# Kernel tuning notes

Hardware: AMD Instinct MI355X
Metric: run time of the kernel (lower is better)

## Reference

```python
import jax, jax.numpy as jnp
import numpy as np

ALPHA = 1.0

def setup_inputs() -> dict:
    key = jax.random.key(0)
    X = jax.random.normal(key, (8192, 64), dtype=jnp.float32)
    return {"X": X}

def reference(X) -> jnp.ndarray:
    # Pairwise squared L2 distances via GEMM trick: ||x_i||^2 + ||x_j||^2 - 2 x_i.x_j
    sq = jnp.sum(X * X, axis=1)                      # [N]
    d2 = sq[:, None] + sq[None, :] - 2.0 * (X @ X.T)  # [N, N]
    d2 = jnp.maximum(d2, 0.0)
    # sigma^2 = alpha * mean(d2), detached (no grad through bandwidth)
    sigma_sq = ALPHA * jax.lax.stop_gradient(jnp.mean(d2))
    return jnp.exp(-d2 / (2.0 * sigma_sq))
```

## Files before the change

kernel.cpp:

```cpp
#include <hip/hip_runtime.h>
#include <hip/hip_bf16.h>

#define N 8192
#define D 64

typedef __attribute__((ext_vector_type(8))) short bf16x8;
typedef __attribute__((ext_vector_type(4))) float f32x4;

__device__ inline unsigned short f2b(float f) {
    __hip_bfloat16 h = __float2bfloat16(f);
    return __builtin_bit_cast(unsigned short, h);
}

__global__ __launch_bounds__(256) void gk_prep(const float4* __restrict__ X4,
                                               ushort4* __restrict__ Xb4,
                                               float* __restrict__ sq,
                                               float4* __restrict__ Vp4) {
    __shared__ float4 sm[256];
    const int tid = threadIdx.x;
    const int g = blockIdx.x * 256 + tid;
    float4 v = X4[g];
    ushort4 b;
    b.x = f2b(v.x); b.y = f2b(v.y); b.z = f2b(v.z); b.w = f2b(v.w);
    Xb4[g] = b;
    float ss = v.x * v.x + v.y * v.y + v.z * v.z + v.w * v.w;
    ss += __shfl_xor(ss, 8, 16);
    ss += __shfl_xor(ss, 4, 16);
    ss += __shfl_xor(ss, 2, 16);
    ss += __shfl_xor(ss, 1, 16);
    if ((tid & 15) == 0) sq[g >> 4] = ss;
    sm[tid] = v;
    __syncthreads();
#pragma unroll
    for (int off = 128; off >= 16; off >>= 1) {
        if (tid < off) {
            float4 o = sm[tid + off];
            float4 m = sm[tid];
            m.x += o.x; m.y += o.y; m.z += o.z; m.w += o.w;
            sm[tid] = m;
        }
        __syncthreads();
    }
    if (tid < 16) Vp4[blockIdx.x * 16 + tid] = sm[tid];
}

__global__ __launch_bounds__(256) void gk_finalize(const float* __restrict__ sq,
                                                   const float* __restrict__ Vp,
                                                   float* __restrict__ scal) {
    __shared__ float red[256];
    const int tid = threadIdx.x;
    float s = 0.f;
    for (int r = tid; r < N; r += 256) s += sq[r];
    red[tid] = s;
    __syncthreads();
    for (int off = 128; off > 0; off >>= 1) {
        if (tid < off) red[tid] += red[tid + off];
        __syncthreads();
    }
    const float S = red[0];
    __syncthreads();
    const int c = tid & 63, p = tid >> 6;
    float v = 0.f;
    for (int r = p; r < 512; r += 4) v += Vp[r * 64 + c];
    red[tid] = v;
    __syncthreads();
    if (tid < 128) red[tid] += red[tid + 128];
    __syncthreads();
    if (tid < 64) red[tid] += red[tid + 64];
    __syncthreads();
    float vv = (tid < 64) ? red[tid] * red[tid] : 0.f;
    __syncthreads();
    red[tid] = vv;
    __syncthreads();
    for (int off = 128; off > 0; off >>= 1) {
        if (tid < off) red[tid] += red[tid + off];
        __syncthreads();
    }
    if (tid == 0) {
        const float Vsq = red[0];
        const float fN = (float)N;
        const float mean = 2.f * S / fN - 2.f * Vsq / (fN * fN);
        scal[0] = 1.f / (2.f * mean);
    }
}

__global__ __launch_bounds__(256) void gk_main(const unsigned short* __restrict__ Xb,
                                               const float* __restrict__ sq,
                                               const float* __restrict__ scal,
                                               float* __restrict__ out) {
    const int lane = threadIdx.x & 63;
    const int wave = threadIdx.x >> 6;
    const int i0 = blockIdx.y * 64 + wave * 16;
    const int j0 = blockIdx.x * 128;
    const int m = lane & 15;
    const int q = lane >> 4;
    const float c0 = scal[0];

    const bf16x8* Brow = reinterpret_cast<const bf16x8*>(Xb + (i0 + m) * D + 8 * q);
    const bf16x8 b0 = Brow[0];
    const bf16x8 b1 = Brow[4];

    f32x4 acc[8];
#pragma unroll
    for (int t = 0; t < 8; ++t) acc[t] = (f32x4){0.f, 0.f, 0.f, 0.f};

#pragma unroll
    for (int t = 0; t < 8; ++t) {
        const bf16x8* Arow =
            reinterpret_cast<const bf16x8*>(Xb + (j0 + t * 16 + m) * D + 8 * q);
        acc[t] = __builtin_amdgcn_mfma_f32_16x16x32_bf16(Arow[0], b0, acc[t], 0, 0, 0);
        acc[t] = __builtin_amdgcn_mfma_f32_16x16x32_bf16(Arow[4], b1, acc[t], 0, 0, 0);
    }

    const float sqi = sq[i0 + m];
    float* orow = out + (size_t)(i0 + m) * N + j0 + 4 * q;
    const f32x4* sq4 = reinterpret_cast<const f32x4*>(sq + j0 + 4 * q);

#pragma unroll
    for (int t = 0; t < 8; ++t) {
        const f32x4 sj = sq4[t * 4];
        f32x4 e;
        e[0] = __expf(-fmaxf(sqi + sj[0] - 2.f * acc[t][0], 0.f) * c0);
        e[1] = __expf(-fmaxf(sqi + sj[1] - 2.f * acc[t][1], 0.f) * c0);
        e[2] = __expf(-fmaxf(sqi + sj[2] - 2.f * acc[t][2], 0.f) * c0);
        e[3] = __expf(-fmaxf(sqi + sj[3] - 2.f * acc[t][3], 0.f) * c0);
        *reinterpret_cast<f32x4*>(orow + t * 16) = e;
    }
}

extern "C" void kernel_launch(void* const* d_in, const int* in_sizes, int n_in,
                              void* d_out, int out_size, void* d_ws, size_t ws_size,
                              hipStream_t stream) {
    const float* X = (const float*)d_in[0];
    float* out = (float*)d_out;

    char* ws = (char*)d_ws;
    unsigned short* Xb = (unsigned short*)ws;
    float* sq = (float*)(ws + (1 << 20));
    float* Vp = (float*)(ws + (1 << 20) + (32 << 10));
    float* scal = (float*)(ws + (1 << 20) + (32 << 10) + (128 << 10));

    gk_prep<<<512, 256, 0, stream>>>((const float4*)X, (ushort4*)Xb, sq, (float4*)Vp);
    gk_finalize<<<1, 256, 0, stream>>>(sq, Vp, scal);

    dim3 grid(N / 128, N / 64);
    gk_main<<<grid, 256, 0, stream>>>(Xb, sq, scal, out);
}
```

Baseline: 342.5 us.

## Stage output tile through LDS for coalesced row stores and fold scale into exp2

Each wave now writes its exp results to a swizzled LDS tile and re-reads it so that each half-wave stores 512 contiguous bytes of one output row, instead of scattered 16-byte stores across 16 rows. Separately, the squared norms are pre-scaled by the bandwidth constant and log2(e) in the finalize kernel, so the epilogue becomes one FMA, a min and a native exp2. The goal is better write coalescing on a kernel bound by its 256MB output and a shorter epilogue, at the cost of 32KB of LDS per block, which may lower occupancy, plus an extra pass over the norms.

```diff
diff --git a/kernel.cpp b/kernel.cpp
--- a/kernel.cpp
+++ b/kernel.cpp
@@ -10,6 +10,14 @@
 __device__ inline unsigned short f2b(float f) {
     __hip_bfloat16 h = __float2bfloat16(f);
     return __builtin_bit_cast(unsigned short, h);
+}
+
+__device__ inline float exp2fast(float x) {
+#if __has_builtin(__builtin_amdgcn_exp2f)
+    return __builtin_amdgcn_exp2f(x);
+#else
+    return exp2f(x);
+#endif
 }
 
 __global__ __launch_bounds__(256) void gk_prep(const float4* __restrict__ X4,
@@ -46,7 +54,8 @@
 
 __global__ __launch_bounds__(256) void gk_finalize(const float* __restrict__ sq,
                                                    const float* __restrict__ Vp,
-                                                   float* __restrict__ scal) {
+                                                   float* __restrict__ scal,
+                                                   float4* __restrict__ u4) {
     __shared__ float red[256];
     const int tid = threadIdx.x;
     float s = 0.f;
@@ -80,21 +89,35 @@
         const float Vsq = red[0];
         const float fN = (float)N;
         const float mean = 2.f * S / fN - 2.f * Vsq / (fN * fN);
-        scal[0] = 1.f / (2.f * mean);
+        const float sc = 1.f / (2.f * mean);
+        const float L2E = 1.4426950408889634f;
+        scal[0] = sc;
+        scal[1] = 2.f * sc * L2E;
+        red[0] = sc * L2E;
+    }
+    __syncthreads();
+    const float uc = red[0];
+    const float4* sqv = reinterpret_cast<const float4*>(sq);
+    for (int r = tid; r < N / 4; r += 256) {
+        float4 q = sqv[r];
+        float4 o;
+        o.x = q.x * uc; o.y = q.y * uc; o.z = q.z * uc; o.w = q.w * uc;
+        u4[r] = o;
     }
 }
 
 __global__ __launch_bounds__(256) void gk_main(const unsigned short* __restrict__ Xb,
-                                               const float* __restrict__ sq,
+                                               const float* __restrict__ u,
                                                const float* __restrict__ scal,
                                                float* __restrict__ out) {
+    __shared__ float lds[4][16][128];
     const int lane = threadIdx.x & 63;
     const int wave = threadIdx.x >> 6;
     const int i0 = blockIdx.y * 64 + wave * 16;
     const int j0 = blockIdx.x * 128;
     const int m = lane & 15;
     const int q = lane >> 4;
-    const float c0 = scal[0];
+    const float k2 = scal[1];
 
     const bf16x8* Brow = reinterpret_cast<const bf16x8*>(Xb + (i0 + m) * D + 8 * q);
     const bf16x8 b0 = Brow[0];
@@ -112,19 +135,32 @@
         acc[t] = __builtin_amdgcn_mfma_f32_16x16x32_bf16(Arow[4], b1, acc[t], 0, 0, 0);
     }
 
-    const float sqi = sq[i0 + m];
-    float* orow = out + (size_t)(i0 + m) * N + j0 + 4 * q;
-    const f32x4* sq4 = reinterpret_cast<const f32x4*>(sq + j0 + 4 * q);
+    const float ui = u[i0 + m];
+    const f32x4* u4 = reinterpret_cast<const f32x4*>(u + j0 + 4 * q);
+    float* ldsrow = &lds[wave][m][0];
 
 #pragma unroll
     for (int t = 0; t < 8; ++t) {
-        const f32x4 sj = sq4[t * 4];
+        const f32x4 uj = u4[t * 4];
         f32x4 e;
-        e[0] = __expf(-fmaxf(sqi + sj[0] - 2.f * acc[t][0], 0.f) * c0);
-        e[1] = __expf(-fmaxf(sqi + sj[1] - 2.f * acc[t][1], 0.f) * c0);
-        e[2] = __expf(-fmaxf(sqi + sj[2] - 2.f * acc[t][2], 0.f) * c0);
-        e[3] = __expf(-fmaxf(sqi + sj[3] - 2.f * acc[t][3], 0.f) * c0);
-        *reinterpret_cast<f32x4*>(orow + t * 16) = e;
+#pragma unroll
+        for (int r = 0; r < 4; ++r) {
+            const float s = ui + uj[r];
+            const float pz = fmaf(k2, acc[t][r], -s);
+            e[r] = exp2fast(fminf(pz, 0.f));
+        }
+        const int cs = (16 * t + 4 * q + 4 * m) & 127;
+        *reinterpret_cast<f32x4*>(ldsrow + cs) = e;
+    }
+
+    const int half = lane >> 5;
+    const int c = (lane & 31) * 4;
+#pragma unroll
+    for (int p = 0; p < 8; ++p) {
+        const int r = 2 * p + half;
+        const int cr = (c + 4 * r) & 127;
+        const f32x4 v = *reinterpret_cast<const f32x4*>(&lds[wave][r][cr]);
+        *reinterpret_cast<f32x4*>(out + (size_t)(i0 + r) * N + j0 + c) = v;
     }
 }
 
@@ -138,11 +174,12 @@
     unsigned short* Xb = (unsigned short*)ws;
     float* sq = (float*)(ws + (1 << 20));
     float* Vp = (float*)(ws + (1 << 20) + (32 << 10));
-    float* scal = (float*)(ws + (1 << 20) + (32 << 10) + (128 << 10));
+    float* u  = (float*)(ws + (1 << 20) + (160 << 10));
+    float* scal = (float*)(ws + (1 << 20) + (192 << 10));
 
     gk_prep<<<512, 256, 0, stream>>>((const float4*)X, (ushort4*)Xb, sq, (float4*)Vp);
-    gk_finalize<<<1, 256, 0, stream>>>(sq, Vp, scal);
+    gk_finalize<<<1, 256, 0, stream>>>(sq, Vp, scal, (float4*)u);
 
     dim3 grid(N / 128, N / 64);
-    gk_main<<<grid, 256, 0, stream>>>(Xb, sq, scal, out);
+    gk_main<<<grid, 256, 0, stream>>>(Xb, u, scal, out);
 }
```

After: 334.4 us. 2.4% less time.
